# Optimization experiments

Hardware: AMD Instinct MI355X
Metric: run time of the kernel (lower is better)

## Reference

```python
import jax, jax.numpy as jnp
import numpy as np

H = 1024      # hidden_size
NH = 16       # num_heads
HD = H // NH  # head_dim
FF = 4 * H    # ffn hidden


def setup_inputs() -> dict:
    key = jax.random.key(0)
    ks = jax.random.split(key, 11)
    s = 1.0 / np.sqrt(H)
    inp = {
        "x": jax.random.normal(ks[0], (2, 2048, H), dtype=jnp.float32),
        "Wq": jax.random.uniform(ks[1], (H, H), jnp.float32, -s, s),
        "Wk": jax.random.uniform(ks[2], (H, H), jnp.float32, -s, s),
        "Wv": jax.random.uniform(ks[3], (H, H), jnp.float32, -s, s),
        "Wo": jax.random.uniform(ks[4], (H, H), jnp.float32, -s, s),
        "ln1_g": jnp.ones((H,), jnp.float32),
        "ln1_b": jnp.zeros((H,), jnp.float32),
        "ln2_g": jnp.ones((H,), jnp.float32),
        "ln2_b": jnp.zeros((H,), jnp.float32),
        "W1": jax.random.uniform(ks[5], (H, FF), jnp.float32, -s, s),
        "b1": jnp.zeros((FF,), jnp.float32),
        "W2": jax.random.uniform(ks[6], (FF, H), jnp.float32, -1.0 / np.sqrt(FF), 1.0 / np.sqrt(FF)),
        "b2": jnp.zeros((H,), jnp.float32),
    }
    return inp


def _layernorm(x, g, b, eps=1e-5):
    mu = jnp.mean(x, axis=-1, keepdims=True)
    var = jnp.mean(jnp.square(x - mu), axis=-1, keepdims=True)
    return (x - mu) * jax.lax.rsqrt(var + eps) * g + b


def reference(x, Wq, Wk, Wv, Wo, ln1_g, ln1_b, ln2_g, ln2_b, W1, b1, W2, b2):
    bsz, seq, _ = x.shape
    h = _layernorm(x, ln1_g, ln1_b)
    # project and split heads: [b, s, H] -> [b, nh, s, hd]
    def split(t):
        return t.reshape(bsz, seq, NH, HD).transpose(0, 2, 1, 3)
    q = split(h @ Wq.T)
    k = split(h @ Wk.T)
    v = split(h @ Wv.T)
    scores = jnp.einsum("bhqd,bhkd->bhqk", q, k) / jnp.sqrt(jnp.float32(HD))
    probs = jax.nn.softmax(scores, axis=-1)
    attn = jnp.einsum("bhqk,bhkd->bhqd", probs, v)
    attn = attn.transpose(0, 2, 1, 3).reshape(bsz, seq, H)
    x = x + attn @ Wo.T
    h2 = _layernorm(x, ln2_g, ln2_b)
    ffn = jax.nn.gelu(h2 @ W1 + b1, approximate=False) @ W2 + b2
    return x + ffn
```

## Files before the change

### kernel.cpp

```cpp
#include <hip/hip_runtime.h>
#include <stdint.h>
#include <math.h>

typedef float f32x4 __attribute__((ext_vector_type(4)));
typedef __bf16 bf16x8 __attribute__((ext_vector_type(8)));

#define DEVI __device__ __forceinline__

#if __has_builtin(__builtin_amdgcn_exp2f)
#define EXP2(x) __builtin_amdgcn_exp2f(x)
#else
#define EXP2(x) exp2f(x)
#endif

#define LOG2E 1.44269504f

DEVI unsigned short f2bf(float f) {
  union { float f; unsigned int u; } c; c.f = f;
  unsigned int u = c.u;
  return (unsigned short)((u + 0x7FFFu + ((u >> 16) & 1u)) >> 16);
}

DEVI unsigned short f2bf_fast(float f) {
  union { float f; unsigned int u; } c; c.f = f;
  return (unsigned short)((c.u + 0x8000u) >> 16);
}

DEVI void gll16(const void* g, void* l) {
  __builtin_amdgcn_global_load_lds(
      (const __attribute__((address_space(1))) void*)g,
      (__attribute__((address_space(3))) void*)l,
      16, 0, 0);
}

__global__ __launch_bounds__(256) void cvt_weights(
    const float* __restrict__ Wq, const float* __restrict__ Wk,
    const float* __restrict__ Wv, const float* __restrict__ Wo,
    unsigned short* __restrict__ WB, unsigned short* __restrict__ WoB) {
  int i = blockIdx.x * 256 + threadIdx.x;
  int seg = i >> 18;
  int j = i & 262143;
  const float* src = (seg == 0) ? Wq : (seg == 1) ? Wk : (seg == 2) ? Wv : Wo;
  unsigned short* dst = (seg < 3) ? WB + (size_t)seg * 1048576 : WoB;
  float4 v = ((const float4*)src)[j];
  ushort4 ov;
  ov.x = f2bf(v.x); ov.y = f2bf(v.y); ov.z = f2bf(v.z); ov.w = f2bf(v.w);
  ((ushort4*)dst)[j] = ov;
}

__global__ __launch_bounds__(256) void transpose_f32_bf16(
    const float* __restrict__ in, unsigned short* __restrict__ out, int R, int C) {
  __shared__ float tile[32][33];
  int bc = blockIdx.x * 32, br = blockIdx.y * 32;
  int tx = threadIdx.x & 31, ty = threadIdx.x >> 5;
#pragma unroll
  for (int i = 0; i < 32; i += 8)
    tile[ty + i][tx] = in[(size_t)(br + ty + i) * C + bc + tx];
  __syncthreads();
#pragma unroll
  for (int i = 0; i < 32; i += 8)
    out[(size_t)(bc + ty + i) * R + br + tx] = f2bf(tile[tx][ty + i]);
}

__global__ __launch_bounds__(256) void vtrans(
    const unsigned short* __restrict__ QKV, unsigned short* __restrict__ Vt) {
  int stile = blockIdx.x;
  int bh = blockIdx.y;
  int b = bh >> 4, h = bh & 15;
  __shared__ unsigned short tile[64][68];
  const unsigned short* src =
      QKV + ((size_t)(b * 2048 + stile * 64)) * 3072 + 2048 + h * 64;
  int t = threadIdx.x;
#pragma unroll
  for (int i = 0; i < 16; i++) {
    int e = i * 256 + t; int s = e >> 6, d = e & 63;
    tile[s][d] = src[(size_t)s * 3072 + d];
  }
  __syncthreads();
  unsigned short* dst = Vt + (size_t)bh * 64 * 2048 + stile * 64;
#pragma unroll
  for (int i = 0; i < 16; i++) {
    int e = i * 256 + t; int d = e >> 6, s = e & 63;
    dst[(size_t)d * 2048 + s] = tile[s][d];
  }
}

__global__ __launch_bounds__(256) void layernorm_bf16(
    const float* __restrict__ x, const float* __restrict__ g,
    const float* __restrict__ be, unsigned short* __restrict__ out) {
  const int row = blockIdx.x;
  const int t = threadIdx.x;
  const float4 v = ((const float4*)(x + (size_t)row * 1024))[t];
  float s = v.x + v.y + v.z + v.w;
  float s2 = v.x * v.x + v.y * v.y + v.z * v.z + v.w * v.w;
#pragma unroll
  for (int d = 32; d > 0; d >>= 1) {
    s += __shfl_down(s, d);
    s2 += __shfl_down(s2, d);
  }
  __shared__ float ps[4], ps2[4], st[2];
  const int lane = t & 63, wave = t >> 6;
  if (lane == 0) { ps[wave] = s; ps2[wave] = s2; }
  __syncthreads();
  if (t == 0) {
    float S = ps[0] + ps[1] + ps[2] + ps[3];
    float S2 = ps2[0] + ps2[1] + ps2[2] + ps2[3];
    float mu = S * (1.0f / 1024.0f);
    float var = S2 * (1.0f / 1024.0f) - mu * mu;
    st[0] = mu; st[1] = rsqrtf(var + 1e-5f);
  }
  __syncthreads();
  float mu = st[0], inv = st[1];
  float4 gv = ((const float4*)g)[t];
  float4 bv = ((const float4*)be)[t];
  ushort4 ov;
  ov.x = f2bf((v.x - mu) * inv * gv.x + bv.x);
  ov.y = f2bf((v.y - mu) * inv * gv.y + bv.y);
  ov.z = f2bf((v.z - mu) * inv * gv.z + bv.z);
  ov.w = f2bf((v.w - mu) * inv * gv.w + bv.w);
  ((ushort4*)(out + (size_t)row * 1024))[t] = ov;
}

DEVI float gelu_f(float x) {
  float a = x * (2.3022082f + 0.1029432f * x * x);
  return x / (1.0f + EXP2(-a));
}

template <int EPI, int TM, int TN>
__global__ __launch_bounds__(256, 4) void gemm_bt(
    const unsigned short* __restrict__ A, const unsigned short* __restrict__ B,
    int M, int N, int K, float* __restrict__ outF, unsigned short* __restrict__ outB,
    const float* __restrict__ res, const float* __restrict__ bias) {
  __shared__ __align__(16) unsigned short As[2][TM * 32];
  __shared__ __align__(16) unsigned short Bs[2][TN * 32];
  constexpr int MF = TM / 32;
  constexpr int NF = TN / 32;
  const int t = threadIdx.x;
  const int lane = t & 63, wave = t >> 6;
  const int wr = wave >> 1, wc = wave & 1;
  const int l15 = lane & 15, lg = lane >> 4;
  const int sl = (t & 7) ^ ((t >> 3) & 7);
  const int srow2 = ((t >> 3) << 1) + (sl >> 2);
  const int scol2 = (sl & 3) * 8;
  const int gx = gridDim.x;
  const int nwg = gx * gridDim.y;
  const int orig = blockIdx.y * gx + blockIdx.x;
  const int swz = (orig & 7) * (nwg >> 3) + (orig >> 3);
  const int bx = swz % gx, by = swz / gx;
  const size_t aBase = (size_t)by * TM * K;
  const size_t bBase = (size_t)bx * TN * K;
  f32x4 acc[MF][NF] = {};

  auto stage = [&](int buf, int kt) {
#pragma unroll
    for (int i = 0; i < TM / 64; i++)
      gll16(A + aBase + (size_t)(srow2 + i * 64) * K + kt + scol2,
            (char*)&As[buf][0] + i * 4096 + t * 16);
#pragma unroll
    for (int i = 0; i < TN / 64; i++)
      gll16(B + bBase + (size_t)(srow2 + i * 64) * K + kt + scol2,
            (char*)&Bs[buf][0] + i * 4096 + t * 16);
  };

  stage(0, 0);
  __syncthreads();
  const int nk = K >> 5;
  for (int ki = 0; ki < nk; ki++) {
    const int cur = ki & 1;
    if (ki + 1 < nk) stage(cur ^ 1, (ki + 1) << 5);
    bf16x8 af[MF], bfv[NF];
#pragma unroll
    for (int m = 0; m < MF; m++) {
      const int R = wr * (TM / 2) + m * 16 + l15;
      const int r = R >> 1;
      const int ps = (((R & 1) << 2) | lg) ^ (r & 7);
      af[m] = *(const bf16x8*)&As[cur][r * 64 + ps * 8];
    }
#pragma unroll
    for (int n = 0; n < NF; n++) {
      const int R = wc * (TN / 2) + n * 16 + l15;
      const int r = R >> 1;
      const int ps = (((R & 1) << 2) | lg) ^ (r & 7);
      bfv[n] = *(const bf16x8*)&Bs[cur][r * 64 + ps * 8];
    }
#pragma unroll
    for (int m = 0; m < MF; m++)
#pragma unroll
      for (int n = 0; n < NF; n++)
        acc[m][n] = __builtin_amdgcn_mfma_f32_16x16x32_bf16(af[m], bfv[n], acc[m][n], 0, 0, 0);
    __syncthreads();
  }
  const int rowB = by * TM + wr * (TM / 2);
  const int colB = bx * TN + wc * (TN / 2);
#pragma unroll
  for (int m = 0; m < MF; m++) {
#pragma unroll
    for (int n = 0; n < NF; n++) {
#pragma unroll
      for (int r = 0; r < 4; r++) {
        int gm = rowB + m * 16 + lg * 4 + r;
        int gn = colB + n * 16 + l15;
        float c = acc[m][n][r];
        size_t idx = (size_t)gm * N + gn;
        if (EPI == 0) {
          outB[idx] = f2bf(c);
        } else if (EPI == 1) {
          outF[idx] = res[idx] + c;
        } else if (EPI == 2) {
          outB[idx] = f2bf(gelu_f(c + bias[gn]));
        } else {
          outF[idx] = res[idx] + c + bias[gn];
        }
      }
    }
  }
}

__global__ __launch_bounds__(512) void attn_flash(
    const unsigned short* __restrict__ QKV, const unsigned short* __restrict__ Vt,
    unsigned short* __restrict__ attnO) {
  __shared__ __align__(16) unsigned short Ks[2][64 * 64];
  __shared__ __align__(16) unsigned short Vs[2][64 * 64];
  __shared__ __align__(16) unsigned short Ps[128 * 64];
  const int t = threadIdx.x;
  const int lane = t & 63, wave = t >> 6;
  const int l15 = lane & 15, lg = lane >> 4;
  const int bid = blockIdx.x;
  const int swzb = (bid & 7) * 64 + (bid >> 3);
  const int qt = swzb & 15;
  const int bh = swzb >> 4;
  const int b = bh >> 4, h = bh & 15;
  const size_t qkvBase = (size_t)b * 2048 * 3072 + (size_t)h * 64;

  bf16x8 aq[2];
  {
    int qrow = qt * 128 + wave * 16 + l15;
    const unsigned short* qp = QKV + qkvBase + (size_t)qrow * 3072;
#pragma unroll
    for (int kc = 0; kc < 2; kc++) {
      aq[kc] = *(const bf16x8*)(qp + kc * 32 + lg * 8);
#pragma unroll
      for (int j = 0; j < 8; j++)
        aq[kc][j] = (__bf16)((float)aq[kc][j] * 0.125f);
    }
  }
  bf16x8 onesf;
#pragma unroll
  for (int j = 0; j < 8; j++) onesf[j] = (__bf16)1.0f;

  const unsigned short* Kg = QKV + qkvBase + 1024;
  const unsigned short* Vg = Vt + (size_t)bh * 64 * 2048;

  f32x4 o[4] = {};
  f32x4 ol = {};
  const float M2 = 4.0f * LOG2E;

  const int srow = t >> 3;
  const int scb = (t & 7) * 16;
  const int e = (scb ^ ((srow & 7) << 4)) >> 1;

  auto stage = [&](int buf, int kt) {
    gll16(Kg + (size_t)(kt * 64 + srow) * 3072 + e, (char*)&Ks[buf][0] + t * 16);
    gll16(Vg + (size_t)srow * 2048 + kt * 64 + e, (char*)&Vs[buf][0] + t * 16);
  };

  stage(0, 0);
  __syncthreads();

  for (int kt = 0; kt < 32; kt++) {
    const int cur = kt & 1;
    if (kt < 31) stage(cur ^ 1, kt + 1);

    f32x4 s[4] = {};
#pragma unroll
    for (int n = 0; n < 4; n++) {
#pragma unroll
      for (int kc = 0; kc < 2; kc++) {
        int r = n * 16 + l15;
        int cb = (kc * 64 + lg * 16) ^ ((r & 7) << 4);
        bf16x8 bk = *(const bf16x8*)&Ks[cur][r * 64 + (cb >> 1)];
        s[n] = __builtin_amdgcn_mfma_f32_16x16x32_bf16(aq[kc], bk, s[n], 0, 0, 0);
      }
    }

    const int q0 = wave * 16 + lg * 4;
#pragma unroll
    for (int n = 0; n < 4; n++)
#pragma unroll
      for (int r = 0; r < 4; r++) {
        int q = q0 + r;
        int cb = ((n * 16 + l15) * 2) ^ ((q & 7) << 4);
        float p = EXP2(__builtin_fmaf(s[n][r], LOG2E, -M2));
        Ps[q * 64 + (cb >> 1)] = f2bf_fast(p);
      }

#pragma unroll
    for (int kc = 0; kc < 2; kc++) {
      int qr = wave * 16 + l15;
      int cbp = (kc * 64 + lg * 16) ^ ((qr & 7) << 4);
      bf16x8 pa = *(const bf16x8*)&Ps[qr * 64 + (cbp >> 1)];
      ol = __builtin_amdgcn_mfma_f32_16x16x32_bf16(pa, onesf, ol, 0, 0, 0);
#pragma unroll
      for (int n = 0; n < 4; n++) {
        int dr = n * 16 + l15;
        int cbv = (kc * 64 + lg * 16) ^ ((dr & 7) << 4);
        bf16x8 bv = *(const bf16x8*)&Vs[cur][dr * 64 + (cbv >> 1)];
        o[n] = __builtin_amdgcn_mfma_f32_16x16x32_bf16(pa, bv, o[n], 0, 0, 0);
      }
    }
    __syncthreads();
  }

  const int qrow0 = qt * 128 + wave * 16;
  unsigned short* op = attnO + ((size_t)(b * 2048 + qrow0)) * 1024 + h * 64;
  float inv[4];
#pragma unroll
  for (int r = 0; r < 4; r++) inv[r] = 1.0f / ol[r];
#pragma unroll
  for (int n = 0; n < 4; n++)
#pragma unroll
    for (int r = 0; r < 4; r++) {
      int q = lg * 4 + r;
      op[(size_t)q * 1024 + n * 16 + l15] = f2bf(o[n][r] * inv[r]);
    }
}

extern "C" void kernel_launch(void* const* d_in, const int* in_sizes, int n_in,
                              void* d_out, int out_size, void* d_ws, size_t ws_size,
                              hipStream_t stream) {
  const float* x = (const float*)d_in[0];
  const float* Wq = (const float*)d_in[1];
  const float* Wk = (const float*)d_in[2];
  const float* Wv = (const float*)d_in[3];
  const float* Wo = (const float*)d_in[4];
  const float* ln1g = (const float*)d_in[5];
  const float* ln1b = (const float*)d_in[6];
  const float* ln2g = (const float*)d_in[7];
  const float* ln2b = (const float*)d_in[8];
  const float* W1 = (const float*)d_in[9];
  const float* b1 = (const float*)d_in[10];
  const float* W2 = (const float*)d_in[11];
  const float* b2 = (const float*)d_in[12];
  float* out = (float*)d_out;

  char* ws = (char*)d_ws;
  size_t off = 0;
  auto alloc = [&](size_t bytes) {
    void* p = ws + off;
    off += (bytes + 255) & ~(size_t)255;
    return p;
  };
  unsigned short* WB = (unsigned short*)alloc(3072ull * 1024 * 2);
  unsigned short* WoB = (unsigned short*)alloc(1024ull * 1024 * 2);
  unsigned short* W1t = (unsigned short*)alloc(4096ull * 1024 * 2);
  unsigned short* W2t = (unsigned short*)alloc(1024ull * 4096 * 2);
  unsigned short* hb = (unsigned short*)alloc(4096ull * 1024 * 2);
  unsigned short* QKV = (unsigned short*)alloc(4096ull * 3072 * 2);
  unsigned short* attnb = (unsigned short*)alloc(4096ull * 1024 * 2);
  unsigned short* Vtb = (unsigned short*)alloc(32ull * 64 * 2048 * 2);
  float* x2 = (float*)alloc(4096ull * 1024 * 4);
  unsigned short* ffnb = QKV;
  unsigned short* h2b = hb;

  cvt_weights<<<4096, 256, 0, stream>>>(Wq, Wk, Wv, Wo, WB, WoB);
  transpose_f32_bf16<<<dim3(128, 32), 256, 0, stream>>>(W1, W1t, 1024, 4096);
  transpose_f32_bf16<<<dim3(32, 128), 256, 0, stream>>>(W2, W2t, 4096, 1024);
  layernorm_bf16<<<4096, 256, 0, stream>>>(x, ln1g, ln1b, hb);
  gemm_bt<0, 128, 128><<<dim3(24, 32), 256, 0, stream>>>(hb, WB, 4096, 3072, 1024,
                                                         nullptr, QKV, nullptr, nullptr);
  vtrans<<<dim3(32, 32), 256, 0, stream>>>(QKV, Vtb);
  attn_flash<<<512, 512, 0, stream>>>(QKV, Vtb, attnb);
  gemm_bt<1, 64, 128><<<dim3(8, 64), 256, 0, stream>>>(attnb, WoB, 4096, 1024, 1024,
                                                       x2, nullptr, x, nullptr);
  layernorm_bf16<<<4096, 256, 0, stream>>>(x2, ln2g, ln2b, h2b);
  gemm_bt<2, 128, 128><<<dim3(32, 32), 256, 0, stream>>>(h2b, W1t, 4096, 4096, 1024,
                                                         nullptr, ffnb, nullptr, b1);
  gemm_bt<3, 64, 128><<<dim3(8, 64), 256, 0, stream>>>(ffnb, W2t, 4096, 1024, 4096,
                                                       out, nullptr, x2, b2);
}
```

Before: 246.3 us.

## Use 512-thread 8-wave GEMM for QKV and FFN-up projections

Adds a gemm_bt8 kernel that covers the same 128x128 output tile with 8 waves (2x4) instead of 4. Each wave holds a 64x32 sub-tile, which halves its accumulator registers, and each thread issues one global-to-LDS load per operand per K step instead of two. The goal is more waves per CU to hide latency in the QKV and W1 GEMMs. The cost is lower MFMA-to-LDS-read reuse per wave and a 512-thread barrier on every K step. The old gemm_bt drops its bf16 epilogues and now keeps only the fp32 residual paths.

Result: no change. 245.7 us (median of 2 runs) (-0.3%).

```diff
diff --git a/kernel.cpp b/kernel.cpp
--- a/kernel.cpp
+++ b/kernel.cpp
@@ -126,10 +126,85 @@
   return x / (1.0f + EXP2(-a));
 }
 
+template <int EPI>
+__global__ __launch_bounds__(512, 4) void gemm_bt8(
+    const unsigned short* __restrict__ A, const unsigned short* __restrict__ B,
+    int M, int N, int K, unsigned short* __restrict__ outB,
+    const float* __restrict__ bias) {
+  __shared__ __align__(16) unsigned short As[2][128 * 32];
+  __shared__ __align__(16) unsigned short Bs[2][128 * 32];
+  const int t = threadIdx.x;
+  const int lane = t & 63, wave = t >> 6;
+  const int wm = wave >> 2, wn = wave & 3;
+  const int l15 = lane & 15, lg = lane >> 4;
+  const int sl = (t & 7) ^ ((t >> 3) & 7);
+  const int srow2 = ((t >> 3) << 1) + (sl >> 2);
+  const int scol2 = (sl & 3) * 8;
+  const int gx = gridDim.x;
+  const int nwg = gx * gridDim.y;
+  const int orig = blockIdx.y * gx + blockIdx.x;
+  const int swz = (orig & 7) * (nwg >> 3) + (orig >> 3);
+  const int bx = swz % gx, by = swz / gx;
+  const size_t aBase = (size_t)by * 128 * K;
+  const size_t bBase = (size_t)bx * 128 * K;
+  f32x4 acc[4][2] = {};
+
+  auto stage = [&](int buf, int kt) {
+    gll16(A + aBase + (size_t)srow2 * K + kt + scol2, (char*)&As[buf][0] + t * 16);
+    gll16(B + bBase + (size_t)srow2 * K + kt + scol2, (char*)&Bs[buf][0] + t * 16);
+  };
+
+  stage(0, 0);
+  __syncthreads();
+  const int nk = K >> 5;
+  for (int ki = 0; ki < nk; ki++) {
+    const int cur = ki & 1;
+    if (ki + 1 < nk) stage(cur ^ 1, (ki + 1) << 5);
+    bf16x8 af[4], bfv[2];
+#pragma unroll
+    for (int m = 0; m < 4; m++) {
+      const int R = wm * 64 + m * 16 + l15;
+      const int r = R >> 1;
+      const int ps = (((R & 1) << 2) | lg) ^ (r & 7);
+      af[m] = *(const bf16x8*)&As[cur][r * 64 + ps * 8];
+    }
+#pragma unroll
+    for (int n = 0; n < 2; n++) {
+      const int R = wn * 32 + n * 16 + l15;
+      const int r = R >> 1;
+      const int ps = (((R & 1) << 2) | lg) ^ (r & 7);
+      bfv[n] = *(const bf16x8*)&Bs[cur][r * 64 + ps * 8];
+    }
+#pragma unroll
+    for (int m = 0; m < 4; m++)
+#pragma unroll
+      for (int n = 0; n < 2; n++)
+        acc[m][n] = __builtin_amdgcn_mfma_f32_16x16x32_bf16(af[m], bfv[n], acc[m][n], 0, 0, 0);
+    __syncthreads();
+  }
+  const int rowB = by * 128 + wm * 64;
+  const int colB = bx * 128 + wn * 32;
+#pragma unroll
+  for (int m = 0; m < 4; m++) {
+#pragma unroll
+    for (int n = 0; n < 2; n++) {
+      const int gn = colB + n * 16 + l15;
+      float bb = (EPI == 2) ? bias[gn] : 0.0f;
+#pragma unroll
+      for (int r = 0; r < 4; r++) {
+        const int gm = rowB + m * 16 + lg * 4 + r;
+        const size_t idx = (size_t)gm * N + gn;
+        if (EPI == 0) outB[idx] = f2bf(acc[m][n][r]);
+        else          outB[idx] = f2bf(gelu_f(acc[m][n][r] + bb));
+      }
+    }
+  }
+}
+
 template <int EPI, int TM, int TN>
 __global__ __launch_bounds__(256, 4) void gemm_bt(
     const unsigned short* __restrict__ A, const unsigned short* __restrict__ B,
-    int M, int N, int K, float* __restrict__ outF, unsigned short* __restrict__ outB,
+    int M, int N, int K, float* __restrict__ outF,
     const float* __restrict__ res, const float* __restrict__ bias) {
   __shared__ __align__(16) unsigned short As[2][TM * 32];
   __shared__ __align__(16) unsigned short Bs[2][TN * 32];
@@ -202,15 +277,8 @@
         int gn = colB + n * 16 + l15;
         float c = acc[m][n][r];
         size_t idx = (size_t)gm * N + gn;
-        if (EPI == 0) {
-          outB[idx] = f2bf(c);
-        } else if (EPI == 1) {
-          outF[idx] = res[idx] + c;
-        } else if (EPI == 2) {
-          outB[idx] = f2bf(gelu_f(c + bias[gn]));
-        } else {
-          outF[idx] = res[idx] + c + bias[gn];
-        }
+        if (EPI == 1) outF[idx] = res[idx] + c;
+        else          outF[idx] = res[idx] + c + bias[gn];
       }
     }
   }
@@ -366,15 +434,15 @@
   transpose_f32_bf16<<<dim3(128, 32), 256, 0, stream>>>(W1, W1t, 1024, 4096);
   transpose_f32_bf16<<<dim3(32, 128), 256, 0, stream>>>(W2, W2t, 4096, 1024);
   layernorm_bf16<<<4096, 256, 0, stream>>>(x, ln1g, ln1b, hb);
-  gemm_bt<0, 128, 128><<<dim3(24, 32), 256, 0, stream>>>(hb, WB, 4096, 3072, 1024,
-                                                         nullptr, QKV, nullptr, nullptr);
+  gemm_bt8<0><<<dim3(24, 32), 512, 0, stream>>>(hb, WB, 4096, 3072, 1024,
+                                                QKV, nullptr);
   vtrans<<<dim3(32, 32), 256, 0, stream>>>(QKV, Vtb);
   attn_flash<<<512, 512, 0, stream>>>(QKV, Vtb, attnb);
   gemm_bt<1, 64, 128><<<dim3(8, 64), 256, 0, stream>>>(attnb, WoB, 4096, 1024, 1024,
-                                                       x2, nullptr, x, nullptr);
+                                                       x2, x, nullptr);
   layernorm_bf16<<<4096, 256, 0, stream>>>(x2, ln2g, ln2b, h2b);
-  gemm_bt<2, 128, 128><<<dim3(32, 32), 256, 0, stream>>>(h2b, W1t, 4096, 4096, 1024,
-                                                         nullptr, ffnb, nullptr, b1);
+  gemm_bt8<2><<<dim3(32, 32), 512, 0, stream>>>(h2b, W1t, 4096, 4096, 1024,
+                                                ffnb, b1);
   gemm_bt<3, 64, 128><<<dim3(8, 64), 256, 0, stream>>>(ffnb, W2t, 4096, 1024, 4096,
-                                                       out, nullptr, x2, b2);
-}
+                                                       out, x2, b2);
+}
```
